# Optimization experiments

Measured on AMD Instinct MI355X. Metric: run time of the kernel, lower is better.

The kernel has to match this reference:

```python
import jax, jax.numpy as jnp
import numpy as np

N_EMBED = 1024
EMBED_DIM = 256

def setup_inputs() -> dict:
    key = jax.random.key(0)
    k1, k2 = jax.random.split(key)
    hidden_states = jax.random.normal(k1, (64, 32, 32, EMBED_DIM), dtype=jnp.float32)
    emb_weights = jax.random.normal(k2, (N_EMBED, EMBED_DIM), dtype=jnp.float32)
    return {"hidden_states": hidden_states, "emb_weights": emb_weights}

def reference(hidden_states, emb_weights):
    # flatten (B,H,W,C) -> (N, C) with C == embed_dim
    z_flat = hidden_states.reshape((-1, EMBED_DIM))
    # squared distance: ||z||^2 + ||e||^2 - 2 z.e
    distance = (
        jnp.sum(z_flat ** 2, axis=1, keepdims=True)
        + jnp.sum(emb_weights ** 2, axis=1)
        - 2.0 * jnp.dot(z_flat, emb_weights.T)
    )  # (N, n_embed)
    min_encoding_indices = jnp.argmin(distance, axis=1)  # (N,)
    z_q = jnp.take(emb_weights, min_encoding_indices, axis=0).reshape(hidden_states.shape)
    min_encoding_indices = min_encoding_indices.reshape(hidden_states.shape[0], -1)
    return z_q, min_encoding_indices
```

## Files before the change

kernel.cpp:

```cpp
#include <hip/hip_runtime.h>

typedef _Float16 half8  __attribute__((ext_vector_type(8)));
typedef _Float16 half4  __attribute__((ext_vector_type(4)));
typedef float    float4v __attribute__((ext_vector_type(4)));
typedef float    float8v __attribute__((ext_vector_type(8)));

#define N_ROWS  65536
#define N_CODES 1024
#define DIM     256
#define BM      128
#define NBLKS   (N_ROWS / BM)

__global__ __launch_bounds__(64)
void vq_prep(const float* __restrict__ emb, float* __restrict__ e_norm,
             _Float16* __restrict__ e_frag) {
    const int c = blockIdx.x, lane = threadIdx.x;
    const int l15 = c & 15, nt = c >> 4;
    float4v v = ((const float4v*)(emb + (size_t)c * DIM))[lane];
    half4 h, l;
    float ss = 0.f;
    #pragma unroll
    for (int j = 0; j < 4; ++j) {
        float x = v[j];
        ss += x * x;
        _Float16 hh = (_Float16)x;
        h[j] = hh;
        l[j] = (_Float16)(x - (float)hh);
    }
    const int ks = lane >> 3, q = (lane >> 1) & 3, jb = (lane & 1) * 4;
    _Float16* p = e_frag + ((size_t)(nt * 8 + ks)) * 1024 + (q * 16 + l15) * 8 + jb;
    *(half4*)p = h;
    *(half4*)(p + 512) = l;
    #pragma unroll
    for (int m = 32; m >= 1; m >>= 1) ss += __shfl_xor(ss, m, 64);
    if (lane == 0) e_norm[c] = ss;
}

__global__ __launch_bounds__(512, 2)
void vq_main(const float* __restrict__ z,
             const _Float16* __restrict__ e_frag,
             const float* __restrict__ e_norm,
             const float* __restrict__ emb,
             float* __restrict__ zq,
             float* __restrict__ idxf,
             int fused_gather) {
    __shared__ _Float16 sA[64 * 2 * 512];
    __shared__ float    s_nrm[N_CODES];
    __shared__ float2   s_best[BM][17];
    __shared__ int      s_idx[BM];

    const int t = threadIdx.x;
    const int w = t >> 6, lane = t & 63, quad = lane >> 4, l15 = lane & 15;
    const int rowblk = blockIdx.x * BM;

    s_nrm[t] = e_norm[t];
    s_nrm[t + 512] = e_norm[t + 512];

    #pragma unroll
    for (int i = 0; i < 8; ++i) {
        const int mt = i, ks = w;
        const int row = mt * 16 + l15;
        const int col = ks * 32 + quad * 8;
        float8v v = *(const float8v*)(z + (size_t)(rowblk + row) * DIM + col);
        half8 h, lo;
        #pragma unroll
        for (int j = 0; j < 8; ++j) {
            float x = v[j];
            _Float16 hh = (_Float16)x;
            h[j] = hh;
            lo[j] = (_Float16)(x - (float)hh);
        }
        _Float16* p = sA + (size_t)((mt * 8 + ks) * 2) * 512 + lane * 8;
        *(half8*)p = h;
        *(half8*)(p + 512) = lo;
    }
    __syncthreads();

    #pragma unroll
    for (int pass = 0; pass < 2; ++pass) {
        const int ntbase = w * 8 + pass * 4;
        float4v acc[8][4] = {};

        for (int ks = 0; ks < 8; ++ks) {
            half8 bh[4], bl[4];
            #pragma unroll
            for (int nt = 0; nt < 4; ++nt) {
                const _Float16* bp = e_frag + ((size_t)((ntbase + nt) * 8 + ks)) * 1024 + lane * 8;
                bh[nt] = *(const half8*)bp;
                bl[nt] = *(const half8*)(bp + 512);
            }
            #pragma unroll
            for (int mt = 0; mt < 8; ++mt) {
                const _Float16* ap = sA + (size_t)((mt * 8 + ks) * 2) * 512 + lane * 8;
                half8 ah = *(const half8*)ap;
                half8 al = *(const half8*)(ap + 512);
                #pragma unroll
                for (int nt = 0; nt < 4; ++nt) {
                    acc[mt][nt] = __builtin_amdgcn_mfma_f32_16x16x32_f16(ah, bh[nt], acc[mt][nt], 0, 0, 0);
                    acc[mt][nt] = __builtin_amdgcn_mfma_f32_16x16x32_f16(ah, bl[nt], acc[mt][nt], 0, 0, 0);
                    acc[mt][nt] = __builtin_amdgcn_mfma_f32_16x16x32_f16(al, bh[nt], acc[mt][nt], 0, 0, 0);
                }
            }
        }

        float nrm[4]; int cg[4];
        #pragma unroll
        for (int nt = 0; nt < 4; ++nt) {
            cg[nt]  = (ntbase + nt) * 16 + l15;
            nrm[nt] = s_nrm[cg[nt]];
        }
        #pragma unroll
        for (int mt = 0; mt < 8; ++mt) {
            #pragma unroll
            for (int r = 0; r < 4; ++r) {
                float bs = 0.f; int bi = 0;
                #pragma unroll
                for (int nt = 0; nt < 4; ++nt) {
                    float s = nrm[nt] - 2.0f * acc[mt][nt][r];
                    if (nt == 0 || s < bs) { bs = s; bi = cg[nt]; }
                }
                #pragma unroll
                for (int m = 1; m < 16; m <<= 1) {
                    float s2 = __shfl_xor(bs, m, 64);
                    int   i2 = __shfl_xor(bi, m, 64);
                    if (s2 < bs || (s2 == bs && i2 < bi)) { bs = s2; bi = i2; }
                }
                if (l15 == 0) {
                    const int row = mt * 16 + quad * 4 + r;
                    float2 pr; pr.x = bs; pr.y = (float)bi;
                    s_best[row][w * 2 + pass] = pr;
                }
            }
        }
    }
    __syncthreads();

    if (t < BM) {
        float2 p0 = s_best[t][0];
        float bs = p0.x, bi = p0.y;
        #pragma unroll
        for (int s = 1; s < 16; ++s) {
            float2 pv = s_best[t][s];
            if (pv.x < bs || (pv.x == bs && pv.y < bi)) { bs = pv.x; bi = pv.y; }
        }
        s_idx[t] = (int)bi;
        idxf[rowblk + t] = bi;
    }

    if (!fused_gather) return;
    __syncthreads();

    const float4v* emb4 = (const float4v*)emb;
    float4v* zq4 = (float4v*)zq;
    const int rr = t >> 2, cb = t & 3;
    const int code = s_idx[rr];
    #pragma unroll
    for (int i = 0; i < 16; ++i) {
        const int chunk = cb + i * 4;
        zq4[(size_t)(rowblk + rr) * 64 + chunk] = emb4[(size_t)code * 64 + chunk];
    }
}

__global__ __launch_bounds__(256)
void vq_gather(const float* __restrict__ emb,
               const float* __restrict__ idxf,
               float* __restrict__ zq) {
    const int tid  = blockIdx.x * 256 + threadIdx.x;
    const int r    = tid >> 6;
    const int lane = tid & 63;
    const int idx  = (int)idxf[r];
    const float4* ep = (const float4*)(emb + (size_t)idx * DIM);
    ((float4*)(zq + (size_t)r * DIM))[lane] = ep[lane];
}

extern "C" void kernel_launch(void* const* d_in, const int* in_sizes, int n_in,
                              void* d_out, int out_size, void* d_ws, size_t ws_size,
                              hipStream_t stream) {
    const float* z   = (const float*)d_in[0];
    const float* emb = (const float*)d_in[1];

    float* zq   = (float*)d_out;
    float* idxf = zq + (size_t)N_ROWS * DIM;

    const size_t need = 4096 + (size_t)N_CODES * DIM * 2 * sizeof(_Float16);
    const int in_ws = (ws_size >= need);
    char* base = in_ws ? (char*)d_ws : (char*)d_out;
    float*    e_norm = (float*)base;
    _Float16* e_frag = (_Float16*)(base + 4096);

    vq_prep<<<N_CODES, 64, 0, stream>>>(emb, e_norm, e_frag);
    vq_main<<<NBLKS, 512, 0, stream>>>(z, e_frag, e_norm, emb, zq, idxf, in_ws);
    if (!in_ws)
        vq_gather<<<(N_ROWS * 64) / 256, 256, 0, stream>>>(emb, idxf, zq);
}
```

Before: 231.1 us.

## Split passes into four narrower tiles with double-buffered codebook fragment prefetch

The codebook tile each wave handles per pass is narrowed from 4 to 2 code tiles, and the loop runs 4 passes instead of 2. This halves the accumulator registers, and the next k-step's B fragments from global memory are prefetched into a double buffer. The MFMA section is wrapped in s_setprio. The per-wave best is now merged across passes in shared memory, which shrinks s_best and the final reduction. The aim is lower register pressure and hidden global load latency, at the cost of reloading A fragments from LDS more often and running an extra read-modify-write on s_best per pass.

Measured after the change: 278.7 us. 1.21x slower.

```diff
diff --git a/kernel.cpp b/kernel.cpp
--- a/kernel.cpp
+++ b/kernel.cpp
@@ -46,7 +46,7 @@
              int fused_gather) {
     __shared__ _Float16 sA[64 * 2 * 512];
     __shared__ float    s_nrm[N_CODES];
-    __shared__ float2   s_best[BM][17];
+    __shared__ float2   s_best[BM][9];
     __shared__ int      s_idx[BM];
 
     const int t = threadIdx.x;
@@ -55,6 +55,17 @@
 
     s_nrm[t] = e_norm[t];
     s_nrm[t + 512] = e_norm[t + 512];
+
+    half8 bh[2][2], bl[2][2];
+    {
+        const int ntbase0 = w * 8;
+        #pragma unroll
+        for (int nt = 0; nt < 2; ++nt) {
+            const _Float16* bp = e_frag + ((size_t)((ntbase0 + nt) * 8 + 0)) * 1024 + lane * 8;
+            bh[0][nt] = *(const half8*)bp;
+            bl[0][nt] = *(const half8*)(bp + 512);
+        }
+    }
 
     #pragma unroll
     for (int i = 0; i < 8; ++i) {
@@ -76,36 +87,50 @@
     }
     __syncthreads();
 
-    #pragma unroll
-    for (int pass = 0; pass < 2; ++pass) {
-        const int ntbase = w * 8 + pass * 4;
-        float4v acc[8][4] = {};
-
+    for (int pass = 0; pass < 4; ++pass) {
+        const int ntbase = w * 8 + pass * 2;
+
+        if (pass) {
+            #pragma unroll
+            for (int nt = 0; nt < 2; ++nt) {
+                const _Float16* bp = e_frag + ((size_t)((ntbase + nt) * 8 + 0)) * 1024 + lane * 8;
+                bh[0][nt] = *(const half8*)bp;
+                bl[0][nt] = *(const half8*)(bp + 512);
+            }
+        }
+
+        float4v acc[8][2] = {};
+
+        #pragma unroll
         for (int ks = 0; ks < 8; ++ks) {
-            half8 bh[4], bl[4];
-            #pragma unroll
-            for (int nt = 0; nt < 4; ++nt) {
-                const _Float16* bp = e_frag + ((size_t)((ntbase + nt) * 8 + ks)) * 1024 + lane * 8;
-                bh[nt] = *(const half8*)bp;
-                bl[nt] = *(const half8*)(bp + 512);
-            }
+            const int cur = ks & 1, nxt = cur ^ 1;
+            if (ks < 7) {
+                #pragma unroll
+                for (int nt = 0; nt < 2; ++nt) {
+                    const _Float16* bp = e_frag + ((size_t)((ntbase + nt) * 8 + (ks + 1))) * 1024 + lane * 8;
+                    bh[nxt][nt] = *(const half8*)bp;
+                    bl[nxt][nt] = *(const half8*)(bp + 512);
+                }
+            }
+            __builtin_amdgcn_s_setprio(1);
             #pragma unroll
             for (int mt = 0; mt < 8; ++mt) {
                 const _Float16* ap = sA + (size_t)((mt * 8 + ks) * 2) * 512 + lane * 8;
                 half8 ah = *(const half8*)ap;
                 half8 al = *(const half8*)(ap + 512);
                 #pragma unroll
-                for (int nt = 0; nt < 4; ++nt) {
-                    acc[mt][nt] = __builtin_amdgcn_mfma_f32_16x16x32_f16(ah, bh[nt], acc[mt][nt], 0, 0, 0);
-                    acc[mt][nt] = __builtin_amdgcn_mfma_f32_16x16x32_f16(ah, bl[nt], acc[mt][nt], 0, 0, 0);
-                    acc[mt][nt] = __builtin_amdgcn_mfma_f32_16x16x32_f16(al, bh[nt], acc[mt][nt], 0, 0, 0);
-                }
-            }
-        }
-
-        float nrm[4]; int cg[4];
-        #pragma unroll
-        for (int nt = 0; nt < 4; ++nt) {
+                for (int nt = 0; nt < 2; ++nt) {
+                    acc[mt][nt] = __builtin_amdgcn_mfma_f32_16x16x32_f16(ah, bh[cur][nt], acc[mt][nt], 0, 0, 0);
+                    acc[mt][nt] = __builtin_amdgcn_mfma_f32_16x16x32_f16(ah, bl[cur][nt], acc[mt][nt], 0, 0, 0);
+                    acc[mt][nt] = __builtin_amdgcn_mfma_f32_16x16x32_f16(al, bh[cur][nt], acc[mt][nt], 0, 0, 0);
+                }
+            }
+            __builtin_amdgcn_s_setprio(0);
+        }
+
+        float nrm[2]; int cg[2];
+        #pragma unroll
+        for (int nt = 0; nt < 2; ++nt) {
             cg[nt]  = (ntbase + nt) * 16 + l15;
             nrm[nt] = s_nrm[cg[nt]];
         }
@@ -113,12 +138,9 @@
         for (int mt = 0; mt < 8; ++mt) {
             #pragma unroll
             for (int r = 0; r < 4; ++r) {
-                float bs = 0.f; int bi = 0;
-                #pragma unroll
-                for (int nt = 0; nt < 4; ++nt) {
-                    float s = nrm[nt] - 2.0f * acc[mt][nt][r];
-                    if (nt == 0 || s < bs) { bs = s; bi = cg[nt]; }
-                }
+                float bs = nrm[0] - 2.0f * acc[mt][0][r]; int bi = cg[0];
+                float s1 = nrm[1] - 2.0f * acc[mt][1][r];
+                if (s1 < bs) { bs = s1; bi = cg[1]; }
                 #pragma unroll
                 for (int m = 1; m < 16; m <<= 1) {
                     float s2 = __shfl_xor(bs, m, 64);
@@ -127,8 +149,16 @@
                 }
                 if (l15 == 0) {
                     const int row = mt * 16 + quad * 4 + r;
-                    float2 pr; pr.x = bs; pr.y = (float)bi;
-                    s_best[row][w * 2 + pass] = pr;
+                    if (pass == 0) {
+                        float2 pr; pr.x = bs; pr.y = (float)bi;
+                        s_best[row][w] = pr;
+                    } else {
+                        float2 pv = s_best[row][w];
+                        if (bs < pv.x) {
+                            float2 pr; pr.x = bs; pr.y = (float)bi;
+                            s_best[row][w] = pr;
+                        }
+                    }
                 }
             }
         }
@@ -139,7 +169,7 @@
         float2 p0 = s_best[t][0];
         float bs = p0.x, bi = p0.y;
         #pragma unroll
-        for (int s = 1; s < 16; ++s) {
+        for (int s = 1; s < 8; ++s) {
             float2 pv = s_best[t][s];
             if (pv.x < bs || (pv.x == bs && pv.y < bi)) { bs = pv.x; bi = pv.y; }
         }
```

## Halve row block to 64, widen per-wave code tile, add MFMA priority

Applied to the files above, without the earlier changes.

Shrinks the per-block row tile from 128 to 64 rows with 4 waves instead of 8. Each wave now covers 4 row tiles by 8 code tiles, 256 codes over two passes, and merges its pass minima in shared memory instead of keeping separate slots. It also wraps the MFMA section in s_setprio and reorders MFMA issue by nt for more independent chains. This trades lower LDS use and better occupancy or scheduling for doubled total reads of the fp16 codebook fragments across blocks.

After: 200.9 us. 13.1% less time.

```diff
diff --git a/kernel.cpp b/kernel.cpp
--- a/kernel.cpp
+++ b/kernel.cpp
@@ -8,7 +8,7 @@
 #define N_ROWS  65536
 #define N_CODES 1024
 #define DIM     256
-#define BM      128
+#define BM      64
 #define NBLKS   (N_ROWS / BM)
 
 __global__ __launch_bounds__(64)
@@ -36,7 +36,7 @@
     if (lane == 0) e_norm[c] = ss;
 }
 
-__global__ __launch_bounds__(512, 2)
+__global__ __launch_bounds__(256, 2)
 void vq_main(const float* __restrict__ z,
              const _Float16* __restrict__ e_frag,
              const float* __restrict__ e_norm,
@@ -44,23 +44,24 @@
              float* __restrict__ zq,
              float* __restrict__ idxf,
              int fused_gather) {
-    __shared__ _Float16 sA[64 * 2 * 512];
+    __shared__ _Float16 sA[32 * 2 * 512];
     __shared__ float    s_nrm[N_CODES];
-    __shared__ float2   s_best[BM][17];
+    __shared__ float2   s_best[BM][5];
     __shared__ int      s_idx[BM];
 
     const int t = threadIdx.x;
     const int w = t >> 6, lane = t & 63, quad = lane >> 4, l15 = lane & 15;
     const int rowblk = blockIdx.x * BM;
 
-    s_nrm[t] = e_norm[t];
+    s_nrm[t]       = e_norm[t];
+    s_nrm[t + 256] = e_norm[t + 256];
     s_nrm[t + 512] = e_norm[t + 512];
+    s_nrm[t + 768] = e_norm[t + 768];
 
     #pragma unroll
     for (int i = 0; i < 8; ++i) {
-        const int mt = i, ks = w;
-        const int row = mt * 16 + l15;
-        const int col = ks * 32 + quad * 8;
+        const int row = w * 16 + l15;
+        const int col = i * 32 + quad * 8;
         float8v v = *(const float8v*)(z + (size_t)(rowblk + row) * DIM + col);
         half8 h, lo;
         #pragma unroll
@@ -70,54 +71,59 @@
             h[j] = hh;
             lo[j] = (_Float16)(x - (float)hh);
         }
-        _Float16* p = sA + (size_t)((mt * 8 + ks) * 2) * 512 + lane * 8;
+        _Float16* p = sA + (size_t)((w * 8 + i) * 2) * 512 + lane * 8;
         *(half8*)p = h;
         *(half8*)(p + 512) = lo;
     }
     __syncthreads();
 
-    #pragma unroll
     for (int pass = 0; pass < 2; ++pass) {
-        const int ntbase = w * 8 + pass * 4;
-        float4v acc[8][4] = {};
-
+        const int ntbase = w * 16 + pass * 8;
+        float4v acc[4][8] = {};
+
+        #pragma unroll
         for (int ks = 0; ks < 8; ++ks) {
-            half8 bh[4], bl[4];
+            half8 bh[8], bl[8];
             #pragma unroll
-            for (int nt = 0; nt < 4; ++nt) {
+            for (int nt = 0; nt < 8; ++nt) {
                 const _Float16* bp = e_frag + ((size_t)((ntbase + nt) * 8 + ks)) * 1024 + lane * 8;
                 bh[nt] = *(const half8*)bp;
                 bl[nt] = *(const half8*)(bp + 512);
             }
+            __builtin_amdgcn_s_setprio(1);
             #pragma unroll
-            for (int mt = 0; mt < 8; ++mt) {
+            for (int mt = 0; mt < 4; ++mt) {
                 const _Float16* ap = sA + (size_t)((mt * 8 + ks) * 2) * 512 + lane * 8;
                 half8 ah = *(const half8*)ap;
                 half8 al = *(const half8*)(ap + 512);
                 #pragma unroll
-                for (int nt = 0; nt < 4; ++nt) {
+                for (int nt = 0; nt < 8; ++nt)
                     acc[mt][nt] = __builtin_amdgcn_mfma_f32_16x16x32_f16(ah, bh[nt], acc[mt][nt], 0, 0, 0);
+                #pragma unroll
+                for (int nt = 0; nt < 8; ++nt)
                     acc[mt][nt] = __builtin_amdgcn_mfma_f32_16x16x32_f16(ah, bl[nt], acc[mt][nt], 0, 0, 0);
+                #pragma unroll
+                for (int nt = 0; nt < 8; ++nt)
                     acc[mt][nt] = __builtin_amdgcn_mfma_f32_16x16x32_f16(al, bh[nt], acc[mt][nt], 0, 0, 0);
-                }
             }
-        }
-
-        float nrm[4]; int cg[4];
-        #pragma unroll
-        for (int nt = 0; nt < 4; ++nt) {
+            __builtin_amdgcn_s_setprio(0);
+        }
+
+        float nrm[8]; int cg[8];
+        #pragma unroll
+        for (int nt = 0; nt < 8; ++nt) {
             cg[nt]  = (ntbase + nt) * 16 + l15;
             nrm[nt] = s_nrm[cg[nt]];
         }
         #pragma unroll
-        for (int mt = 0; mt < 8; ++mt) {
+        for (int mt = 0; mt < 4; ++mt) {
             #pragma unroll
             for (int r = 0; r < 4; ++r) {
-                float bs = 0.f; int bi = 0;
-                #pragma unroll
-                for (int nt = 0; nt < 4; ++nt) {
+                float bs = nrm[0] - 2.0f * acc[mt][0][r]; int bi = cg[0];
+                #pragma unroll
+                for (int nt = 1; nt < 8; ++nt) {
                     float s = nrm[nt] - 2.0f * acc[mt][nt][r];
-                    if (nt == 0 || s < bs) { bs = s; bi = cg[nt]; }
+                    if (s < bs) { bs = s; bi = cg[nt]; }
                 }
                 #pragma unroll
                 for (int m = 1; m < 16; m <<= 1) {
@@ -127,8 +133,16 @@
                 }
                 if (l15 == 0) {
                     const int row = mt * 16 + quad * 4 + r;
-                    float2 pr; pr.x = bs; pr.y = (float)bi;
-                    s_best[row][w * 2 + pass] = pr;
+                    if (pass == 0) {
+                        float2 pr; pr.x = bs; pr.y = (float)bi;
+                        s_best[row][w] = pr;
+                    } else {
+                        float2 pv = s_best[row][w];
+                        if (bs < pv.x) {
+                            float2 pr; pr.x = bs; pr.y = (float)bi;
+                            s_best[row][w] = pr;
+                        }
+                    }
                 }
             }
         }
@@ -139,7 +153,7 @@
         float2 p0 = s_best[t][0];
         float bs = p0.x, bi = p0.y;
         #pragma unroll
-        for (int s = 1; s < 16; ++s) {
+        for (int s = 1; s < 4; ++s) {
             float2 pv = s_best[t][s];
             if (pv.x < bs || (pv.x == bs && pv.y < bi)) { bs = pv.x; bi = pv.y; }
         }
@@ -189,7 +203,7 @@
     _Float16* e_frag = (_Float16*)(base + 4096);
 
     vq_prep<<<N_CODES, 64, 0, stream>>>(emb, e_norm, e_frag);
-    vq_main<<<NBLKS, 512, 0, stream>>>(z, e_frag, e_norm, emb, zq, idxf, in_ws);
+    vq_main<<<NBLKS, 256, 0, stream>>>(z, e_frag, e_norm, emb, zq, idxf, in_ws);
     if (!in_ws)
         vq_gather<<<(N_ROWS * 64) / 256, 256, 0, stream>>>(emb, idxf, zq);
 }
```
